# Optimization experiments

Measured on AMD Instinct MI355X. Metric: run time of the kernel, lower is better.

Reference implementation:

```python
import jax, jax.numpy as jnp
import numpy as np

B, L, D, U = 8, 512, 256, 32

def setup_inputs() -> dict:
    key = jax.random.key(0)
    ks = jax.random.split(key, 6)
    g = lambda k, shape: jax.random.normal(k, shape, dtype=jnp.float32) * (2.0 / sum(shape)) ** 0.5
    return {
        "x": jax.random.normal(ks[0], (B, L, D), dtype=jnp.float32),
        "Wt": g(ks[1], (D, U)),
        "Wx": g(ks[2], (D, U)),
        "bh": jnp.zeros((U,), dtype=jnp.float32),
        "Wa": g(ks[3], (U, 1)),
        "ba": jnp.zeros((1,), dtype=jnp.float32),
    }

def reference(x, Wt, Wx, bh, Wa, ba):
    # q: [B,L,1,U], k: [B,1,L,U]
    q = jnp.einsum('bld,du->blu', x, Wt)[:, :, None, :]
    k = jnp.einsum('bld,du->blu', x, Wx)[:, None, :, :]
    beta = jnp.tanh(q + k + bh)                      # [B,L,L,U]
    alpha = jnp.einsum('bstu,u->bst', beta, Wa[:, 0]) + ba[0]  # [B,L,L]
    a = jax.nn.softmax(alpha, axis=-1)               # softmax over keys
    c_r = jnp.einsum('bst,btd->bsd', a, x)           # [B,L,D]
    return c_r
```

## Files before the change

kernel.cpp:

```cpp
#include <hip/hip_runtime.h>

#define B 8
#define L 512
#define D 256
#define U 32
#define ST 8
#define QKR 8

__device__ __forceinline__ float tanh_pade(float z) {
    z = fminf(fmaxf(z, -4.97f), 4.97f);
    float s = z * z;
    float p = fmaf(s, fmaf(s, s + 378.f, 17325.f), 135135.f) * z;
    float q = fmaf(s, fmaf(s, fmaf(s, 28.f, 3150.f), 62370.f), 135135.f);
    return p * __builtin_amdgcn_rcpf(q);
}

__global__ __launch_bounds__(256) void qk_kernel(
    const float* __restrict__ x,
    const float* __restrict__ Wt,
    const float* __restrict__ Wx,
    const float* __restrict__ bh,
    float* __restrict__ qb,
    float* __restrict__ kk)
{
    __shared__ float  xs[QKR][D + 1];
    __shared__ float4 pq[3][QKR][8];
    __shared__ float4 pk[3][QKR][8];

    const int row0 = blockIdx.x * QKR;
    const int tid  = threadIdx.x;

    const float4* xg = (const float4*)(x + row0 * D);
    #pragma unroll
    for (int i = tid; i < QKR * D / 4; i += 256) {
        float4 v = xg[i];
        int r = i >> 6;
        int c = (i & 63) << 2;
        xs[r][c] = v.x; xs[r][c + 1] = v.y; xs[r][c + 2] = v.z; xs[r][c + 3] = v.w;
    }
    __syncthreads();

    const int dq = tid >> 6;
    const int r  = (tid >> 3) & 7;
    const int g  = tid & 7;
    const float4* __restrict__ Wt4 = (const float4*)Wt;
    const float4* __restrict__ Wx4 = (const float4*)Wx;

    float4 qa = {0.f, 0.f, 0.f, 0.f};
    float4 ka = {0.f, 0.f, 0.f, 0.f};
    const int d0 = dq * (D / 4);
    #pragma unroll 8
    for (int dd = 0; dd < D / 4; ++dd) {
        const int d = d0 + dd;
        float  xv = xs[r][d];
        float4 wt = Wt4[d * 8 + g];
        float4 wx = Wx4[d * 8 + g];
        qa.x = fmaf(xv, wt.x, qa.x); qa.y = fmaf(xv, wt.y, qa.y);
        qa.z = fmaf(xv, wt.z, qa.z); qa.w = fmaf(xv, wt.w, qa.w);
        ka.x = fmaf(xv, wx.x, ka.x); ka.y = fmaf(xv, wx.y, ka.y);
        ka.z = fmaf(xv, wx.z, ka.z); ka.w = fmaf(xv, wx.w, ka.w);
    }

    if (dq > 0) { pq[dq - 1][r][g] = qa; pk[dq - 1][r][g] = ka; }
    __syncthreads();
    if (dq == 0) {
        #pragma unroll
        for (int w = 0; w < 3; ++w) {
            float4 a = pq[w][r][g], b = pk[w][r][g];
            qa.x += a.x; qa.y += a.y; qa.z += a.z; qa.w += a.w;
            ka.x += b.x; ka.y += b.y; ka.z += b.z; ka.w += b.w;
        }
        float4 b4 = ((const float4*)bh)[g];
        qa.x += b4.x; qa.y += b4.y; qa.z += b4.z; qa.w += b4.w;
        const int row = row0 + r;
        ((float4*)qb)[row * 8 + g] = qa;
        ((float4*)kk)[row * 8 + g] = ka;
    }
}

__global__ __launch_bounds__(512) void attn_kernel(
    const float* __restrict__ x,
    const float* __restrict__ qb,
    const float* __restrict__ kk,
    const float* __restrict__ Wa,
    const float* __restrict__ ba,
    float* __restrict__ out)
{
    const int blk = blockIdx.x;
    const int b   = blk >> 6;
    const int s0  = (blk & 63) * ST;
    const int tid = threadIdx.x;

    __shared__ float  a_sh[ST][L];
    __shared__ float4 part[7][ST][64];

    const float  ba0  = ba[0];
    const float* __restrict__ qrow = qb + (b * L + s0) * U;
    const float* __restrict__ kb   = kk + b * L * U;

    {
        const int t = tid;
        float kv[U];
        const float4* k4 = (const float4*)(kb + t * U);
        #pragma unroll
        for (int c = 0; c < 8; ++c) {
            float4 v = k4[c];
            kv[4 * c] = v.x; kv[4 * c + 1] = v.y; kv[4 * c + 2] = v.z; kv[4 * c + 3] = v.w;
        }
        #pragma unroll 1
        for (int s = 0; s < ST; ++s) {
            const float* __restrict__ q = qrow + s * U;
            float acc = ba0;
            #pragma unroll
            for (int u = 0; u < U; ++u)
                acc = fmaf(tanh_pade(q[u] + kv[u]), Wa[u], acc);
            a_sh[s][t] = acc;
        }
    }
    __syncthreads();

    {
        const int s = tid >> 6, ln = tid & 63;
        float v[8];
        #pragma unroll
        for (int j = 0; j < 8; ++j) v[j] = a_sh[s][ln + 64 * j];
        float m = v[0];
        #pragma unroll
        for (int j = 1; j < 8; ++j) m = fmaxf(m, v[j]);
        #pragma unroll
        for (int off = 1; off < 64; off <<= 1) m = fmaxf(m, __shfl_xor(m, off));
        float e[8], sum = 0.f;
        #pragma unroll
        for (int j = 0; j < 8; ++j) { e[j] = __expf(v[j] - m); sum += e[j]; }
        #pragma unroll
        for (int off = 1; off < 64; off <<= 1) sum += __shfl_xor(sum, off);
        float inv = 1.f / sum;
        #pragma unroll
        for (int j = 0; j < 8; ++j) a_sh[s][ln + 64 * j] = e[j] * inv;
    }
    __syncthreads();

    const int tq = tid >> 6;
    const int dg = tid & 63;
    const float4* __restrict__ x4 = (const float4*)(x + b * L * D);

    float4 acc[ST];
    #pragma unroll
    for (int s = 0; s < ST; ++s) acc[s] = make_float4(0.f, 0.f, 0.f, 0.f);

    #pragma unroll 2
    for (int jj = 0; jj < 16; ++jj) {
        const int tj = tq * 16 + jj;
        float4 av[ST];
        #pragma unroll
        for (int s = 0; s < ST; ++s) av[s] = ((const float4*)a_sh[s])[tj];
        #pragma unroll
        for (int c = 0; c < 4; ++c) {
            const int t = 4 * tj + c;
            float4 xv = x4[t * 64 + dg];
            #pragma unroll
            for (int s = 0; s < ST; ++s) {
                float a = (c == 0) ? av[s].x : (c == 1) ? av[s].y : (c == 2) ? av[s].z : av[s].w;
                acc[s].x = fmaf(a, xv.x, acc[s].x);
                acc[s].y = fmaf(a, xv.y, acc[s].y);
                acc[s].z = fmaf(a, xv.z, acc[s].z);
                acc[s].w = fmaf(a, xv.w, acc[s].w);
            }
        }
    }

    if (tq > 0) {
        #pragma unroll
        for (int s = 0; s < ST; ++s) part[tq - 1][s][dg] = acc[s];
    }
    __syncthreads();
    if (tq == 0) {
        float4* __restrict__ out4 = (float4*)out;
        #pragma unroll
        for (int s = 0; s < ST; ++s) {
            float4 r = acc[s];
            #pragma unroll
            for (int w = 0; w < 7; ++w) {
                float4 p = part[w][s][dg];
                r.x += p.x; r.y += p.y; r.z += p.z; r.w += p.w;
            }
            out4[(b * L + s0 + s) * 64 + dg] = r;
        }
    }
}

extern "C" void kernel_launch(void* const* d_in, const int* in_sizes, int n_in,
                              void* d_out, int out_size, void* d_ws, size_t ws_size,
                              hipStream_t stream)
{
    const float* x  = (const float*)d_in[0];
    const float* Wt = (const float*)d_in[1];
    const float* Wx = (const float*)d_in[2];
    const float* bh = (const float*)d_in[3];
    const float* Wa = (const float*)d_in[4];
    const float* ba = (const float*)d_in[5];
    float* out = (float*)d_out;

    float* qb = (float*)d_ws;
    float* kk = qb + B * L * U;

    qk_kernel<<<B * L / QKR, 256, 0, stream>>>(x, Wt, Wx, bh, qb, kk);
    attn_kernel<<<B * (L / ST), 512, 0, stream>>>(x, qb, kk, Wa, ba, out);
}
```

Measured before the change: 132.4 us.

## Use exp2-based tanh identity, keep scores in registers, broadcast weights via readlane

```diff
diff --git a/kernel.cpp b/kernel.cpp
--- a/kernel.cpp
+++ b/kernel.cpp
@@ -7,13 +7,8 @@
 #define ST 8
 #define QKR 8
 
-__device__ __forceinline__ float tanh_pade(float z) {
-    z = fminf(fmaxf(z, -4.97f), 4.97f);
-    float s = z * z;
-    float p = fmaf(s, fmaf(s, s + 378.f, 17325.f), 135135.f) * z;
-    float q = fmaf(s, fmaf(s, fmaf(s, 28.f, 3150.f), 62370.f), 135135.f);
-    return p * __builtin_amdgcn_rcpf(q);
-}
+#define K2E    2.885390081777927f
+#define KLOG2E 1.4426950408889634f
 
 __global__ __launch_bounds__(256) void qk_kernel(
     const float* __restrict__ x,
@@ -27,7 +22,9 @@
     __shared__ float4 pq[3][QKR][8];
     __shared__ float4 pk[3][QKR][8];
 
-    const int row0 = blockIdx.x * QKR;
+    const int b    = blockIdx.x & 7;
+    const int tile = blockIdx.x >> 3;
+    const int row0 = b * L + tile * QKR;
     const int tid  = threadIdx.x;
 
     const float4* xg = (const float4*)(x + row0 * D);
@@ -66,9 +63,9 @@
     if (dq == 0) {
         #pragma unroll
         for (int w = 0; w < 3; ++w) {
-            float4 a = pq[w][r][g], b = pk[w][r][g];
+            float4 a = pq[w][r][g], c = pk[w][r][g];
             qa.x += a.x; qa.y += a.y; qa.z += a.z; qa.w += a.w;
-            ka.x += b.x; ka.y += b.y; ka.z += b.z; ka.w += b.w;
+            ka.x += c.x; ka.y += c.y; ka.z += c.z; ka.w += c.w;
         }
         float4 b4 = ((const float4*)bh)[g];
         qa.x += b4.x; qa.y += b4.y; qa.z += b4.z; qa.w += b4.w;
@@ -76,6 +73,10 @@
         ((float4*)qb)[row * 8 + g] = qa;
         ((float4*)kk)[row * 8 + g] = ka;
     }
+}
+
+__device__ __forceinline__ float bcast(float v, int lane) {
+    return __int_as_float(__builtin_amdgcn_readlane(__float_as_int(v), lane));
 }
 
 __global__ __launch_bounds__(512) void attn_kernel(
@@ -87,104 +88,148 @@
     float* __restrict__ out)
 {
     const int blk = blockIdx.x;
-    const int b   = blk >> 6;
-    const int s0  = (blk & 63) * ST;
+    const int b   = blk & 7;
+    const int s0  = (blk >> 3) * ST;
     const int tid = threadIdx.x;
-
-    __shared__ float  a_sh[ST][L];
+    const int wv  = tid >> 6;
+    const int ln  = tid & 63;
+
     __shared__ float4 part[7][ST][64];
-
-    const float  ba0  = ba[0];
-    const float* __restrict__ qrow = qb + (b * L + s0) * U;
-    const float* __restrict__ kb   = kk + b * L * U;
-
-    {
-        const int t = tid;
-        float kv[U];
-        const float4* k4 = (const float4*)(kb + t * U);
+    __shared__ float  redm[ST][8];
+    __shared__ float  reds[ST][8];
+
+    float kv[U];
+    {
+        const float4* k4 = (const float4*)(kk + (b * L + tid) * U);
         #pragma unroll
         for (int c = 0; c < 8; ++c) {
             float4 v = k4[c];
-            kv[4 * c] = v.x; kv[4 * c + 1] = v.y; kv[4 * c + 2] = v.z; kv[4 * c + 3] = v.w;
-        }
-        #pragma unroll 1
+            kv[4*c]   = v.x * K2E; kv[4*c+1] = v.y * K2E;
+            kv[4*c+2] = v.z * K2E; kv[4*c+3] = v.w * K2E;
+        }
+    }
+    float wa2[U], sWa = 0.f;
+    {
+        const float4* w4 = (const float4*)Wa;
+        #pragma unroll
+        for (int c = 0; c < 8; ++c) {
+            float4 v = w4[c];
+            wa2[4*c]   = v.x * (-2.f * KLOG2E);
+            wa2[4*c+1] = v.y * (-2.f * KLOG2E);
+            wa2[4*c+2] = v.z * (-2.f * KLOG2E);
+            wa2[4*c+3] = v.w * (-2.f * KLOG2E);
+            sWa += (v.x + v.y) + (v.z + v.w);
+        }
+    }
+    const float base = (sWa + ba[0]) * KLOG2E;
+
+    const float* __restrict__ qrow = qb + (b * L + s0) * U;
+    float avK[ST];
+    #pragma unroll 1
+    for (int s = 0; s < ST; ++s) {
+        const float* __restrict__ q = qrow + s * U;
+        float acc = base;
+        #pragma unroll
+        for (int u = 0; u < U; ++u) {
+            float z = fmaf(q[u], K2E, kv[u]);
+            float e = __builtin_amdgcn_exp2f(z);
+            float r = __builtin_amdgcn_rcpf(e + 1.f);
+            acc = fmaf(r, wa2[u], acc);
+        }
+        avK[s] = acc;
+    }
+
+    {
+        float mw0,mw1,mw2,mw3,mw4,mw5,mw6,mw7;
+        float m[ST];
+        #pragma unroll
         for (int s = 0; s < ST; ++s) {
-            const float* __restrict__ q = qrow + s * U;
-            float acc = ba0;
-            #pragma unroll
-            for (int u = 0; u < U; ++u)
-                acc = fmaf(tanh_pade(q[u] + kv[u]), Wa[u], acc);
-            a_sh[s][t] = acc;
-        }
-    }
-    __syncthreads();
-
-    {
-        const int s = tid >> 6, ln = tid & 63;
-        float v[8];
-        #pragma unroll
-        for (int j = 0; j < 8; ++j) v[j] = a_sh[s][ln + 64 * j];
-        float m = v[0];
-        #pragma unroll
-        for (int j = 1; j < 8; ++j) m = fmaxf(m, v[j]);
-        #pragma unroll
-        for (int off = 1; off < 64; off <<= 1) m = fmaxf(m, __shfl_xor(m, off));
-        float e[8], sum = 0.f;
-        #pragma unroll
-        for (int j = 0; j < 8; ++j) { e[j] = __expf(v[j] - m); sum += e[j]; }
-        #pragma unroll
-        for (int off = 1; off < 64; off <<= 1) sum += __shfl_xor(sum, off);
-        float inv = 1.f / sum;
-        #pragma unroll
-        for (int j = 0; j < 8; ++j) a_sh[s][ln + 64 * j] = e[j] * inv;
-    }
-    __syncthreads();
-
-    const int tq = tid >> 6;
-    const int dg = tid & 63;
+            float v = avK[s];
+            #pragma unroll
+            for (int off = 1; off < 64; off <<= 1) v = fmaxf(v, __shfl_xor(v, off));
+            m[s] = v;
+        }
+        mw0=m[0];mw1=m[1];mw2=m[2];mw3=m[3];mw4=m[4];mw5=m[5];mw6=m[6];mw7=m[7];
+        if (ln == 0) {
+            redm[0][wv]=mw0; redm[1][wv]=mw1; redm[2][wv]=mw2; redm[3][wv]=mw3;
+            redm[4][wv]=mw4; redm[5][wv]=mw5; redm[6][wv]=mw6; redm[7][wv]=mw7;
+        }
+    }
+    __syncthreads();
+    float ew[ST];
+    {
+        float sm[ST];
+        #pragma unroll
+        for (int s = 0; s < ST; ++s) {
+            float gm = redm[s][0];
+            #pragma unroll
+            for (int w = 1; w < 8; ++w) gm = fmaxf(gm, redm[s][w]);
+            float e = __builtin_amdgcn_exp2f(avK[s] - gm);
+            ew[s] = e;
+            float ss = e;
+            #pragma unroll
+            for (int off = 1; off < 64; off <<= 1) ss += __shfl_xor(ss, off);
+            sm[s] = ss;
+        }
+        if (ln == 0) {
+            reds[0][wv]=sm[0]; reds[1][wv]=sm[1]; reds[2][wv]=sm[2]; reds[3][wv]=sm[3];
+            reds[4][wv]=sm[4]; reds[5][wv]=sm[5]; reds[6][wv]=sm[6]; reds[7][wv]=sm[7];
+        }
+    }
+    __syncthreads();
+    float inv[ST];
+    #pragma unroll
+    for (int s = 0; s < ST; ++s) {
+        float ss = reds[s][0];
+        #pragma unroll
+        for (int w = 1; w < 8; ++w) ss += reds[s][w];
+        inv[s] = __builtin_amdgcn_rcpf(ss);
+    }
+
     const float4* __restrict__ x4 = (const float4*)(x + b * L * D);
+    const int tbase = wv * 64;
 
     float4 acc[ST];
     #pragma unroll
     for (int s = 0; s < ST; ++s) acc[s] = make_float4(0.f, 0.f, 0.f, 0.f);
 
-    #pragma unroll 2
-    for (int jj = 0; jj < 16; ++jj) {
-        const int tj = tq * 16 + jj;
-        float4 av[ST];
-        #pragma unroll
-        for (int s = 0; s < ST; ++s) av[s] = ((const float4*)a_sh[s])[tj];
+    #pragma unroll 1
+    for (int j = 0; j < 64; j += 4) {
+        float4 xv[4];
+        #pragma unroll
+        for (int c = 0; c < 4; ++c)
+            xv[c] = x4[(tbase + j + c) * 64 + ln];
         #pragma unroll
         for (int c = 0; c < 4; ++c) {
-            const int t = 4 * tj + c;
-            float4 xv = x4[t * 64 + dg];
             #pragma unroll
             for (int s = 0; s < ST; ++s) {
-                float a = (c == 0) ? av[s].x : (c == 1) ? av[s].y : (c == 2) ? av[s].z : av[s].w;
-                acc[s].x = fmaf(a, xv.x, acc[s].x);
-                acc[s].y = fmaf(a, xv.y, acc[s].y);
-                acc[s].z = fmaf(a, xv.z, acc[s].z);
-                acc[s].w = fmaf(a, xv.w, acc[s].w);
+                float a = bcast(ew[s], j + c);
+                acc[s].x = fmaf(a, xv[c].x, acc[s].x);
+                acc[s].y = fmaf(a, xv[c].y, acc[s].y);
+                acc[s].z = fmaf(a, xv[c].z, acc[s].z);
+                acc[s].w = fmaf(a, xv[c].w, acc[s].w);
             }
         }
     }
 
-    if (tq > 0) {
-        #pragma unroll
-        for (int s = 0; s < ST; ++s) part[tq - 1][s][dg] = acc[s];
-    }
-    __syncthreads();
-    if (tq == 0) {
+    if (wv > 0) {
+        #pragma unroll
+        for (int s = 0; s < ST; ++s) part[wv - 1][s][ln] = acc[s];
+    }
+    __syncthreads();
+    if (wv == 0) {
         float4* __restrict__ out4 = (float4*)out;
         #pragma unroll
         for (int s = 0; s < ST; ++s) {
             float4 r = acc[s];
             #pragma unroll
             for (int w = 0; w < 7; ++w) {
-                float4 p = part[w][s][dg];
+                float4 p = part[w][s][ln];
                 r.x += p.x; r.y += p.y; r.z += p.z; r.w += p.w;
             }
-            out4[(b * L + s0 + s) * 64 + dg] = r;
+            const float iv = inv[s];
+            r.x *= iv; r.y *= iv; r.z *= iv; r.w *= iv;
+            out4[(b * L + s0 + s) * 64 + ln] = r;
         }
     }
 }
```

New measurement: 121.5 us. -8.2%, faster.
